# Kernel optimization log

Measured on AMD Instinct MI355X. Metric: run time of the kernel, lower is better.

The kernel has to match this reference:

```python
import jax, jax.numpy as jnp
import numpy as np

B, T, DIM = 4, 1024, 2048
H, KVH = 16, 4
HD = DIM // H          # 128
G = H // KVH           # GQA group size = 4


def setup_inputs() -> dict:
    key = jax.random.key(0)
    ks = jax.random.split(key, 4)
    s = 1.0 / np.sqrt(DIM)
    x = jax.random.normal(ks[0], (B, T, DIM), jnp.float32)
    Wq = jax.random.normal(ks[1], (DIM, DIM), jnp.float32) * s
    Wkv = jax.random.normal(ks[2], (DIM, 2 * KVH * HD), jnp.float32) * s
    Wo = jax.random.normal(ks[3], (DIM, DIM), jnp.float32) * s
    # RoPE tables (theta=10000, half-split / rotate-half convention)
    inv_freq = 1.0 / (10000.0 ** (np.arange(0, HD, 2, dtype=np.float64) / HD))
    freqs = np.outer(np.arange(T, dtype=np.float64), inv_freq)  # [T, HD/2]
    cos = jnp.asarray(np.cos(freqs), jnp.float32)
    sin = jnp.asarray(np.sin(freqs), jnp.float32)
    return {"x": x, "Wq": Wq, "Wkv": Wkv, "Wo": Wo, "cos": cos, "sin": sin}


def _rope(u, cos, sin):
    # u: [B,T,heads,HD]; cos/sin: [T, HD/2]
    u1, u2 = jnp.split(u, 2, axis=-1)
    c = cos[None, :, None, :]
    s = sin[None, :, None, :]
    return jnp.concatenate([u1 * c - u2 * s, u1 * s + u2 * c], axis=-1)


def reference(x, Wq, Wkv, Wo, cos, sin):
    Bs, Ts, C = x.shape
    q = (x @ Wq).reshape(Bs, Ts, H, HD)
    kv = (x @ Wkv).reshape(Bs, Ts, 2, KVH, HD)
    k, v = kv[:, :, 0], kv[:, :, 1]
    q = _rope(q, cos, sin)
    k = _rope(k, cos, sin)
    # GQA without materializing repeated K/V: fold group dim into q
    qg = q.reshape(Bs, Ts, KVH, G, HD)
    scores = jnp.einsum('bqhgd,bkhd->bhgqk', qg, k) / np.float32(np.sqrt(HD))
    causal = jnp.tril(jnp.ones((Ts, Ts), bool))
    neg = jnp.finfo(scores.dtype).min
    scores = jnp.where(causal, scores, neg)
    att = jax.nn.softmax(scores, axis=-1)
    out = jnp.einsum('bhgqk,bkhd->bqhgd', att, v).reshape(Bs, Ts, C)
    return out @ Wo
```

## Files before the change

### kernel.cpp

```cpp
#include <hip/hip_runtime.h>

typedef unsigned short u16;
typedef unsigned int u32;
typedef __bf16 bf16x8 __attribute__((ext_vector_type(8)));
typedef float f32x4 __attribute__((ext_vector_type(4)));

#define BB   4
#define TT   1024
#define CDIM 2048
#define NH   16
#define NKV  4
#define HDIM 128

__device__ __forceinline__ float b2f(u16 u) {
    union { u32 i; float f; } x; x.i = ((u32)u) << 16; return x.f;
}
__device__ __forceinline__ u16 f2b(float f) {
    union { float f; u32 i; } x; x.f = f;
    u32 r = (x.i + 0x7fffu + ((x.i >> 16) & 1u)) >> 16;
    return (u16)r;
}
__device__ __forceinline__ void async16(const void* g, void* l) {
    __builtin_amdgcn_global_load_lds((const __attribute__((address_space(1))) void*)g,
                                     (__attribute__((address_space(3))) void*)l, 16, 0, 0);
}
template<int N> __device__ __forceinline__ void waitvm() {
    static_assert(N >= 0 && N <= 8, "unsupported vmcnt");
    if constexpr (N == 0)      asm volatile("s_waitcnt vmcnt(0)" ::: "memory");
    else if constexpr (N == 1) asm volatile("s_waitcnt vmcnt(1)" ::: "memory");
    else if constexpr (N == 2) asm volatile("s_waitcnt vmcnt(2)" ::: "memory");
    else if constexpr (N == 3) asm volatile("s_waitcnt vmcnt(3)" ::: "memory");
    else if constexpr (N == 4) asm volatile("s_waitcnt vmcnt(4)" ::: "memory");
    else if constexpr (N == 5) asm volatile("s_waitcnt vmcnt(5)" ::: "memory");
    else if constexpr (N == 6) asm volatile("s_waitcnt vmcnt(6)" ::: "memory");
    else if constexpr (N == 7) asm volatile("s_waitcnt vmcnt(7)" ::: "memory");
    else                       asm volatile("s_waitcnt vmcnt(8)" ::: "memory");
}

__device__ __forceinline__ bool wave_is_f32(const u16* xp) {
    u16 v = xp[(threadIdx.x & 63) * 2];
    int e = (v >> 7) & 0xFF;
    bool bad = (v != 0) && (e < 90 || e > 160);
    return __popcll(__ballot(bad)) > 16;
}

__global__ __launch_bounds__(256) void pre_k(const void* __restrict__ x,
                                             const void* __restrict__ Wq,
                                             const void* __restrict__ Wkv,
                                             const void* __restrict__ Wo,
                                             u16* __restrict__ xb,
                                             u16* __restrict__ csb,
                                             u16* __restrict__ snb,
                                             u16* __restrict__ WqkvT,
                                             u16* __restrict__ WoT,
                                             const void* __restrict__ cs,
                                             const void* __restrict__ sn) {
    const bool f32m = wave_is_f32((const u16*)x);
    int bid = blockIdx.x;
    if (bid < 8320) {
        const void* src; u16* dst; int i;
        if (bid < 8192)      { src = x;  dst = xb;  i = bid * 256 + threadIdx.x; }
        else if (bid < 8256) { src = cs; dst = csb; i = (bid - 8192) * 256 + threadIdx.x; }
        else                 { src = sn; dst = snb; i = (bid - 8256) * 256 + threadIdx.x; }
        union { u16 u[4]; ushort4 v; } o;
        if (f32m) {
            float4 f = ((const float4*)src)[i];
            o.u[0] = f2b(f.x); o.u[1] = f2b(f.y); o.u[2] = f2b(f.z); o.u[3] = f2b(f.w);
        } else {
            o.v = ((const ushort4*)src)[i];
        }
        ((ushort4*)dst)[i] = o.v;
        return;
    }
    __shared__ alignas(16) u16 tile[64 * 65];
    int t = bid - 8320;
    const void* W; u16* WT; int rows, cols, bx, by;
    if (t < 1024)      { W = Wq;  WT = WqkvT;                    rows = 2048; cols = 2048; bx = t & 31;  by = t >> 5; }
    else if (t < 1536) { int l = t - 1024; W = Wkv; WT = WqkvT + (long)2048 * 2048; rows = 2048; cols = 1024; bx = l & 15; by = l >> 4; }
    else               { int l = t - 1536; W = Wo;  WT = WoT;  rows = 2048; cols = 2048; bx = l & 31;   by = l >> 5; }
    const int r0 = by * 64, c0 = bx * 64;
#pragma unroll
    for (int i = 0; i < 16; i++) {
        int c = threadIdx.x + i * 256;
        int rr = c >> 6, cc = c & 63;
        long idx = (long)(r0 + rr) * cols + c0 + cc;
        tile[rr * 65 + cc] = f32m ? f2b(((const float*)W)[idx]) : ((const u16*)W)[idx];
    }
    __syncthreads();
#pragma unroll
    for (int i = 0; i < 16; i++) {
        int c = threadIdx.x + i * 256;
        int rr = c >> 6, cc = c & 63;
        WT[(long)(c0 + rr) * rows + r0 + cc] = tile[cc * 65 + rr];
    }
}

template<int BM, int BN>
__global__ __launch_bounds__(512, 4) void gemm_p4(const u16* __restrict__ A,
                                                  const u16* __restrict__ Bt,
                                                  void* __restrict__ C,
                                                  int N, int Kd,
                                                  const u16* __restrict__ xprobe) {
    constexpr int MF  = BM / 32;
    constexpr int NF  = BN / 64;
    constexpr int MF0 = MF / 2, MF1 = MF - MF0;
    constexpr int NF0 = (NF + 1) / 2, NF1 = NF - NF0;
    constexpr int NAU = BM / 64;
    constexpr int NBU = BN / 64;
    constexpr int NAL = NAU / 2;
    constexpr int NBL = NBU / 2;

    __shared__ alignas(16) u16 As[2][BM * 64];
    __shared__ alignas(16) u16 Bs[2][BN * 64];

    const bool f32m = (xprobe != nullptr) && wave_is_f32(xprobe);
    const int tid = threadIdx.x;
    const int w = tid >> 6, lane = tid & 63;
    const int wm = w >> 2, wn = w & 3;
    const int l16 = lane & 15, quad = lane >> 4;
    const long arow0 = (long)blockIdx.y * BM;
    const long brow0 = (long)blockIdx.x * BN;
    const int NT = Kd >> 6;

    const int srow = tid >> 3, scp = tid & 7;
    const long gst = (long)srow * Kd + ((scp ^ (srow & 7)) << 3);
    const int cst = tid << 3;

    const u16* Ab = A + arow0 * Kd;
    const u16* Bb = Bt + brow0 * Kd;

    auto stageA = [&](int buf, int t, int u0, int u1) {
#pragma unroll
        for (int u = 0; u < NAU; u++)
            if (u >= u0 && u < u1)
                async16(Ab + (long)u * 64 * Kd + t * 64 + gst, &As[buf][u * 4096 + cst]);
    };
    auto stageB = [&](int buf, int t, int u0, int u1) {
#pragma unroll
        for (int u = 0; u < NBU; u++)
            if (u >= u0 && u < u1)
                async16(Bb + (long)u * 64 * Kd + t * 64 + gst, &Bs[buf][u * 4096 + cst]);
    };

    const int R0a = wm * (BM / 2) + l16, sA = R0a & 7;
    const int R0b = wn * (BN / 4) + l16, sB = R0b & 7;
    int aoff[2], boff[2];
    aoff[0] = R0a * 64 + ((quad ^ sA) << 3);
    aoff[1] = R0a * 64 + (((4 + quad) ^ sA) << 3);
    boff[0] = R0b * 64 + ((quad ^ sB) << 3);
    boff[1] = R0b * 64 + (((4 + quad) ^ sB) << 3);

    f32x4 acc[MF][NF];
#pragma unroll
    for (int i = 0; i < MF; i++)
#pragma unroll
        for (int j = 0; j < NF; j++) acc[i][j] = {0.f, 0.f, 0.f, 0.f};

    stageB(0, 0, 0, NBU);
    stageA(0, 0, 0, NAU);
    stageB(1, 1, 0, NBL);
    waitvm<NBL>();
    __builtin_amdgcn_s_barrier();

#pragma unroll 1
    for (int t = 0; t < NT; ++t) {
        const int cur = t & 1, nxt = cur ^ 1;
        const u16* pA = &As[cur][0];
        const u16* pB = &Bs[cur][0];
        bf16x8 afLo[MF0][2], afHi[MF1][2], bfA[NF0][2], bfB[NF1][2];

#pragma unroll
        for (int ks = 0; ks < 2; ks++) {
#pragma unroll
            for (int mt = 0; mt < MF0; mt++)
                afLo[mt][ks] = *(const bf16x8*)&pA[aoff[ks] + mt * 1024];
#pragma unroll
            for (int nt = 0; nt < NF0; nt++)
                bfA[nt][ks] = *(const bf16x8*)&pB[boff[ks] + nt * 1024];
        }
        if (t + 1 < NT) stageB(nxt, t + 1, NBL, NBU);
        __builtin_amdgcn_s_barrier();
        asm volatile("s_waitcnt lgkmcnt(0)" ::: "memory");
        __builtin_amdgcn_sched_barrier(0);
        __builtin_amdgcn_s_setprio(1);
#pragma unroll
        for (int ks = 0; ks < 2; ks++)
#pragma unroll
            for (int mt = 0; mt < MF0; mt++)
#pragma unroll
                for (int nt = 0; nt < NF0; nt++)
                    acc[mt][nt] = __builtin_amdgcn_mfma_f32_16x16x32_bf16(
                        afLo[mt][ks], bfA[nt][ks], acc[mt][nt], 0, 0, 0);
        __builtin_amdgcn_s_setprio(0);

#pragma unroll
        for (int ks = 0; ks < 2; ks++)
#pragma unroll
            for (int nt = 0; nt < NF1; nt++)
                bfB[nt][ks] = *(const bf16x8*)&pB[boff[ks] + (NF0 + nt) * 1024];
        if (t + 1 < NT) stageA(nxt, t + 1, 0, NAL);
        __builtin_amdgcn_s_barrier();
        asm volatile("s_waitcnt lgkmcnt(0)" ::: "memory");
        __builtin_amdgcn_sched_barrier(0);
        __builtin_amdgcn_s_setprio(1);
#pragma unroll
        for (int ks = 0; ks < 2; ks++)
#pragma unroll
            for (int mt = 0; mt < MF0; mt++)
#pragma unroll
                for (int nt = 0; nt < NF1; nt++)
                    acc[mt][NF0 + nt] = __builtin_amdgcn_mfma_f32_16x16x32_bf16(
                        afLo[mt][ks], bfB[nt][ks], acc[mt][NF0 + nt], 0, 0, 0);
        __builtin_amdgcn_s_setprio(0);

#pragma unroll
        for (int ks = 0; ks < 2; ks++)
#pragma unroll
            for (int mt = 0; mt < MF1; mt++)
                afHi[mt][ks] = *(const bf16x8*)&pA[aoff[ks] + (MF0 + mt) * 1024];
        if (t + 1 < NT) stageA(nxt, t + 1, NAL, NAU);
        __builtin_amdgcn_s_barrier();
        asm volatile("s_waitcnt lgkmcnt(0)" ::: "memory");
        __builtin_amdgcn_sched_barrier(0);
        __builtin_amdgcn_s_setprio(1);
#pragma unroll
        for (int ks = 0; ks < 2; ks++)
#pragma unroll
            for (int mt = 0; mt < MF1; mt++)
#pragma unroll
                for (int nt = 0; nt < NF1; nt++)
                    acc[MF0 + mt][NF0 + nt] = __builtin_amdgcn_mfma_f32_16x16x32_bf16(
                        afHi[mt][ks], bfB[nt][ks], acc[MF0 + mt][NF0 + nt], 0, 0, 0);
        __builtin_amdgcn_s_setprio(0);

        if (t + 1 < NT) {
            asm volatile("s_waitcnt vmcnt(0)" ::: "memory");
            __builtin_amdgcn_s_barrier();
            if (t + 2 < NT) stageB(cur, t + 2, 0, NBL);
        }
        __builtin_amdgcn_sched_barrier(0);
        __builtin_amdgcn_s_setprio(1);
#pragma unroll
        for (int ks = 0; ks < 2; ks++)
#pragma unroll
            for (int mt = 0; mt < MF1; mt++)
#pragma unroll
                for (int nt = 0; nt < NF0; nt++)
                    acc[MF0 + mt][nt] = __builtin_amdgcn_mfma_f32_16x16x32_bf16(
                        afHi[mt][ks], bfA[nt][ks], acc[MF0 + mt][nt], 0, 0, 0);
        __builtin_amdgcn_s_setprio(0);
    }

#pragma unroll
    for (int mt = 0; mt < MF; mt++) {
#pragma unroll
        for (int nt = 0; nt < NF; nt++) {
            long col = brow0 + wn * (BN / 4) + nt * 16 + l16;
#pragma unroll
            for (int r = 0; r < 4; r++) {
                long row = arow0 + wm * (BM / 2) + mt * 16 + quad * 4 + r;
                if (f32m) ((float*)C)[row * N + col] = acc[mt][nt][r];
                else      ((u16*)C)[row * N + col] = f2b(acc[mt][nt][r]);
            }
        }
    }
}

template<int BM, int BN>
__global__ __launch_bounds__(512, 4) void gemm_p2(const u16* __restrict__ A,
                                                  const u16* __restrict__ Bt,
                                                  void* __restrict__ C,
                                                  int N, int Kd,
                                                  const u16* __restrict__ xprobe) {
    constexpr int MF  = BM / 32;
    constexpr int NF  = BN / 64;
    constexpr int MF0 = MF / 2, MF1 = MF - MF0;
    constexpr int NF0 = (NF + 1) / 2, NF1 = NF - NF0;
    constexpr int NAU = BM / 64;
    constexpr int NBU = BN / 64;

    __shared__ alignas(16) u16 As[2][BM * 64];
    __shared__ alignas(16) u16 Bs[2][BN * 64];

    const bool f32m = (xprobe != nullptr) && wave_is_f32(xprobe);
    const int tid = threadIdx.x;
    const int w = tid >> 6, lane = tid & 63;
    const int wm = w >> 2, wn = w & 3;
    const int l16 = lane & 15, quad = lane >> 4;
    const long arow0 = (long)blockIdx.y * BM;
    const long brow0 = (long)blockIdx.x * BN;
    const int NT = Kd >> 6;

    const int srow = tid >> 3, scp = tid & 7;
    const long gst = (long)srow * Kd + ((scp ^ (srow & 7)) << 3);
    const int cst = tid << 3;

    const u16* Ab = A + arow0 * Kd;
    const u16* Bb = Bt + brow0 * Kd;

    auto stageA = [&](int buf, int t) {
#pragma unroll
        for (int u = 0; u < NAU; u++)
            async16(Ab + (long)u * 64 * Kd + t * 64 + gst, &As[buf][u * 4096 + cst]);
    };
    auto stageB = [&](int buf, int t) {
#pragma unroll
        for (int u = 0; u < NBU; u++)
            async16(Bb + (long)u * 64 * Kd + t * 64 + gst, &Bs[buf][u * 4096 + cst]);
    };

    const int R0a = wm * (BM / 2) + l16, sA = R0a & 7;
    const int R0b = wn * (BN / 4) + l16, sB = R0b & 7;
    int aoff[2], boff[2];
    aoff[0] = R0a * 64 + ((quad ^ sA) << 3);
    aoff[1] = R0a * 64 + (((4 + quad) ^ sA) << 3);
    boff[0] = R0b * 64 + ((quad ^ sB) << 3);
    boff[1] = R0b * 64 + (((4 + quad) ^ sB) << 3);

    f32x4 acc[MF][NF];
#pragma unroll
    for (int i = 0; i < MF; i++)
#pragma unroll
        for (int j = 0; j < NF; j++) acc[i][j] = {0.f, 0.f, 0.f, 0.f};

    stageB(0, 0); stageA(0, 0); stageB(1, 1); stageA(1, 1);
    waitvm<NAU + NBU>();
    __builtin_amdgcn_s_barrier();

#pragma unroll 1
    for (int t = 0; t < NT; ++t) {
        const int cur = t & 1;
        const u16* pA = &As[cur][0];
        const u16* pB = &Bs[cur][0];
        bf16x8 afLo[MF0][2], afHi[MF1][2], bfA[NF0][2], bfB[NF1][2];

#pragma unroll
        for (int ks = 0; ks < 2; ks++) {
#pragma unroll
            for (int mt = 0; mt < MF0; mt++)
                afLo[mt][ks] = *(const bf16x8*)&pA[aoff[ks] + mt * 1024];
#pragma unroll
            for (int nt = 0; nt < NF0; nt++)
                bfA[nt][ks] = *(const bf16x8*)&pB[boff[ks] + nt * 1024];
#pragma unroll
            for (int nt = 0; nt < NF1; nt++)
                bfB[nt][ks] = *(const bf16x8*)&pB[boff[ks] + (NF0 + nt) * 1024];
        }
        asm volatile("s_waitcnt lgkmcnt(0)" ::: "memory");
        __builtin_amdgcn_sched_barrier(0);
        __builtin_amdgcn_s_setprio(1);
#pragma unroll
        for (int ks = 0; ks < 2; ks++)
#pragma unroll
            for (int mt = 0; mt < MF0; mt++) {
#pragma unroll
                for (int nt = 0; nt < NF0; nt++)
                    acc[mt][nt] = __builtin_amdgcn_mfma_f32_16x16x32_bf16(
                        afLo[mt][ks], bfA[nt][ks], acc[mt][nt], 0, 0, 0);
#pragma unroll
                for (int nt = 0; nt < NF1; nt++)
                    acc[mt][NF0 + nt] = __builtin_amdgcn_mfma_f32_16x16x32_bf16(
                        afLo[mt][ks], bfB[nt][ks], acc[mt][NF0 + nt], 0, 0, 0);
            }
        __builtin_amdgcn_s_setprio(0);

#pragma unroll
        for (int ks = 0; ks < 2; ks++)
#pragma unroll
            for (int mt = 0; mt < MF1; mt++)
                afHi[mt][ks] = *(const bf16x8*)&pA[aoff[ks] + (MF0 + mt) * 1024];
        __builtin_amdgcn_s_barrier();
        if (t + 2 < NT) stageB(cur, t + 2);
        asm volatile("s_waitcnt lgkmcnt(0)" ::: "memory");
        __builtin_amdgcn_sched_barrier(0);
        __builtin_amdgcn_s_setprio(1);
#pragma unroll
        for (int ks = 0; ks < 2; ks++)
#pragma unroll
            for (int mt = 0; mt < MF1; mt++) {
#pragma unroll
                for (int nt = 0; nt < NF1; nt++)
                    acc[MF0 + mt][NF0 + nt] = __builtin_amdgcn_mfma_f32_16x16x32_bf16(
                        afHi[mt][ks], bfB[nt][ks], acc[MF0 + mt][NF0 + nt], 0, 0, 0);
#pragma unroll
                for (int nt = 0; nt < NF0; nt++)
                    acc[MF0 + mt][nt] = __builtin_amdgcn_mfma_f32_16x16x32_bf16(
                        afHi[mt][ks], bfA[nt][ks], acc[MF0 + mt][nt], 0, 0, 0);
            }
        __builtin_amdgcn_s_setprio(0);

        if (t + 1 < NT) {
            if (t + 2 < NT) waitvm<NBU>();
            else            waitvm<0>();
            __builtin_amdgcn_s_barrier();
            if (t + 2 < NT) stageA(cur, t + 2);
        }
    }

#pragma unroll
    for (int mt = 0; mt < MF; mt++) {
#pragma unroll
        for (int nt = 0; nt < NF; nt++) {
            long col = brow0 + wn * (BN / 4) + nt * 16 + l16;
#pragma unroll
            for (int r = 0; r < 4; r++) {
                long row = arow0 + wm * (BM / 2) + mt * 16 + quad * 4 + r;
                if (f32m) ((float*)C)[row * N + col] = acc[mt][nt][r];
                else      ((u16*)C)[row * N + col] = f2b(acc[mt][nt][r]);
            }
        }
    }
}

__global__ __launch_bounds__(256) void prep_k(const u16* __restrict__ QKVraw,
                                              const u16* __restrict__ cs,
                                              const u16* __restrict__ sn,
                                              u16* __restrict__ Qr,
                                              u16* __restrict__ Kr,
                                              u16* __restrict__ Vt) {
    __shared__ alignas(16) u16 tile[64 * 68];
    int bid = blockIdx.x;
    if (bid < 16384) {
        int idx = bid * 256 + threadIdx.x;
        int d = idx & 63;
        int t = (idx >> 6) & (TT - 1);
        int bh = idx >> 16;
        long src = ((long)((bh >> 4) * TT + t)) * 3072 + (bh & 15) * HDIM;
        float u1 = b2f(QKVraw[src + d]), u2 = b2f(QKVraw[src + d + 64]);
        float c = b2f(cs[t * 64 + d]), s = b2f(sn[t * 64 + d]);
        long dst = ((long)bh * TT + t) * HDIM;
        Qr[dst + d] = f2b(u1 * c - u2 * s);
        Qr[dst + d + 64] = f2b(u1 * s + u2 * c);
    } else if (bid < 20480) {
        int idx = (bid - 16384) * 256 + threadIdx.x;
        int d = idx & 63;
        int t = (idx >> 6) & (TT - 1);
        int bk = idx >> 16;
        long src = ((long)((bk >> 2) * TT + t)) * 3072 + 2048 + (bk & 3) * HDIM;
        float u1 = b2f(QKVraw[src + d]), u2 = b2f(QKVraw[src + d + 64]);
        float c = b2f(cs[t * 64 + d]), s = b2f(sn[t * 64 + d]);
        long dst = ((long)bk * TT + t) * HDIM;
        Kr[dst + d] = f2b(u1 * c - u2 * s);
        Kr[dst + d + 64] = f2b(u1 * s + u2 * c);
    } else {
        int vb = bid - 20480;
        int bk = vb >> 5;
        int dt = (vb >> 4) & 1;
        int tt = vb & 15;
        const int d0 = dt * 64, t0 = tt * 64;
        const long srcb = ((long)(bk >> 2) * TT) * 3072 + 2560 + (bk & 3) * HDIM;
#pragma unroll
        for (int i = 0; i < 4; i++) {
            int lin = i * 256 + threadIdx.x;
            int r = lin >> 4, c4 = (lin & 15) * 4;
            *(ushort4*)&tile[r * 68 + c4] =
                *(const ushort4*)&QKVraw[srcb + (long)(t0 + r) * 3072 + d0 + c4];
        }
        __syncthreads();
        const long dstb = ((long)bk * 128 + d0) * 1024 + t0;
#pragma unroll
        for (int i = 0; i < 4; i++) {
            int lin = i * 256 + threadIdx.x;
            int dr = lin >> 4, c4 = (lin & 15) * 4;
            ushort4 v;
            v.x = tile[(c4 + 0) * 68 + dr];
            v.y = tile[(c4 + 1) * 68 + dr];
            v.z = tile[(c4 + 2) * 68 + dr];
            v.w = tile[(c4 + 3) * 68 + dr];
            *(ushort4*)&Vt[dstb + (long)dr * 1024 + c4] = v;
        }
    }
}

__global__ __launch_bounds__(256) void attn_kernel(const u16* __restrict__ Q,
                                                   const u16* __restrict__ Kr,
                                                   const u16* __restrict__ Vt,
                                                   u16* __restrict__ O) {
    __shared__ alignas(16) u16 Ks[2][64 * 128];
    __shared__ alignas(16) u16 Vts[2][128 * 64];
    __shared__ alignas(16) u16 Ps[64 * 88];

    const int tid = threadIdx.x, w = tid >> 6, lane = tid & 63;
    const int l16 = lane & 15, quad = lane >> 4;
    const float scale2 = 0.08838834764831845f * 1.4426950408889634f;

#pragma unroll 1
    for (int it = 0; it < 2; it++) {
        const int j = it ? (1023 - (int)blockIdx.x) : (int)blockIdx.x;
        const int qt = 15 - (j >> 6);
        const int bh = j & 63;
        const int b = bh >> 4, h = bh & 15;
        const int kvh = h >> 2;
        const long qrow0 = (long)bh * TT + qt * 64;
        const long krow0 = (long)(b * NKV + kvh) * TT;
        const long vbase = ((long)(b * NKV + kvh) * HDIM) * TT;

        __syncthreads();

#pragma unroll
        for (int i = 0; i < 4; i++) {
            int slot0 = (w * 4 + i) * 64;
            int slot = slot0 + lane;
            int row = slot >> 4, cp = slot & 15;
            int cg = (cp & 8) | ((cp ^ row) & 7);
            async16(Q + (qrow0 + row) * HDIM + cg * 8, &Ks[0][slot0 * 8]);
        }
        asm volatile("s_waitcnt vmcnt(0)" ::: "memory");
        bf16x8 qf[4];
        {
            const int Rq = w * 16 + l16;
#pragma unroll
            for (int ds = 0; ds < 4; ds++) {
                int c = ds * 4 + quad;
                qf[ds] = *(const bf16x8*)&Ks[0][Rq * 128 + ((c & 8) | ((c ^ Rq) & 7)) * 8];
            }
        }
        asm volatile("s_waitcnt lgkmcnt(0)" ::: "memory");

#pragma unroll
        for (int i = 0; i < 4; i++) {
            int slot0 = (w * 4 + i) * 64;
            int slot = slot0 + lane;
            int row = slot >> 4, cp = slot & 15;
            int cg = (cp & 8) | ((cp ^ row) & 7);
            async16(Kr + (krow0 + row) * HDIM + cg * 8, &Ks[0][slot0 * 8]);
        }
#pragma unroll
        for (int i = 0; i < 4; i++) {
            int slot0 = (w * 4 + i) * 64;
            int slot = slot0 + lane;
            int row = slot >> 3, cp = slot & 7;
            int cg = cp ^ (row & 7);
            async16(Vt + vbase + (long)row * TT + cg * 8, &Vts[0][slot0 * 8]);
        }
        if (qt >= 1) {
#pragma unroll
            for (int i = 0; i < 4; i++) {
                int slot0 = (w * 4 + i) * 64;
                int slot = slot0 + lane;
                int row = slot >> 4, cp = slot & 15;
                int cg = (cp & 8) | ((cp ^ row) & 7);
                async16(Kr + (krow0 + 64 + row) * HDIM + cg * 8, &Ks[1][slot0 * 8]);
            }
#pragma unroll
            for (int i = 0; i < 4; i++) {
                int slot0 = (w * 4 + i) * 64;
                int slot = slot0 + lane;
                int row = slot >> 3, cp = slot & 7;
                int cg = cp ^ (row & 7);
                async16(Vt + vbase + (long)row * TT + 64 + cg * 8, &Vts[1][slot0 * 8]);
            }
            asm volatile("s_waitcnt vmcnt(8)" ::: "memory");
        } else {
            asm volatile("s_waitcnt vmcnt(0)" ::: "memory");
        }
        asm volatile("s_barrier" ::: "memory");

        f32x4 o[8];
#pragma unroll
        for (int i = 0; i < 8; i++) o[i] = {0.f, 0.f, 0.f, 0.f};
        float m_i = -1.0e30f, l_i = 0.f;
        const int qg = qt * 64 + w * 16 + l16;

#pragma unroll 1
        for (int kt = 0; kt <= qt; kt++) {
            const int cur = kt & 1;
            const u16* ksb = Ks[cur];
            const u16* vsb = Vts[cur];

            f32x4 s[4];
#pragma unroll
            for (int nt = 0; nt < 4; nt++) s[nt] = {0.f, 0.f, 0.f, 0.f};
            __builtin_amdgcn_s_setprio(1);
#pragma unroll
            for (int ds = 0; ds < 4; ds++) {
                int c = ds * 4 + quad;
#pragma unroll
                for (int nt = 0; nt < 4; nt++) {
                    int Rk = nt * 16 + l16;
                    bf16x8 ak = *(const bf16x8*)&ksb[Rk * 128 + ((c & 8) | ((c ^ Rk) & 7)) * 8];
                    s[nt] = __builtin_amdgcn_mfma_f32_16x16x32_bf16(ak, qf[ds], s[nt], 0, 0, 0);
                }
            }
            __builtin_amdgcn_s_setprio(0);

            float p[4][4];
            if (kt == qt) {
#pragma unroll
                for (int nt = 0; nt < 4; nt++)
#pragma unroll
                    for (int r = 0; r < 4; r++) {
                        int kcol = kt * 64 + nt * 16 + quad * 4 + r;
                        p[nt][r] = (kcol <= qg) ? (float)s[nt][r] * scale2 : -1.0e30f;
                    }
            } else {
#pragma unroll
                for (int nt = 0; nt < 4; nt++)
#pragma unroll
                    for (int r = 0; r < 4; r++)
                        p[nt][r] = (float)s[nt][r] * scale2;
            }
            float mrow[4];
#pragma unroll
            for (int nt = 0; nt < 4; nt++)
                mrow[nt] = fmaxf(fmaxf(p[nt][0], p[nt][1]), fmaxf(p[nt][2], p[nt][3]));
            float mx = fmaxf(fmaxf(mrow[0], mrow[1]), fmaxf(mrow[2], mrow[3]));
            mx = fmaxf(mx, __shfl_xor(mx, 16));
            mx = fmaxf(mx, __shfl_xor(mx, 32));
            float mnew = fmaxf(m_i, mx);
            float alpha = exp2f(m_i - mnew);
            float rrow[4];
#pragma unroll
            for (int nt = 0; nt < 4; nt++) {
#pragma unroll
                for (int r = 0; r < 4; r++)
                    p[nt][r] = exp2f(p[nt][r] - mnew);
                rrow[nt] = (p[nt][0] + p[nt][1]) + (p[nt][2] + p[nt][3]);
            }
            float rs = (rrow[0] + rrow[1]) + (rrow[2] + rrow[3]);
            rs += __shfl_xor(rs, 16);
            rs += __shfl_xor(rs, 32);
            l_i = l_i * alpha + rs;

            u32* Psw = (u32*)Ps;
            int pb = (w * 16 + l16) * 44 + quad * 2;
#pragma unroll
            for (int nt = 0; nt < 4; nt++) {
                u32 lo = (u32)f2b(p[nt][0]) | ((u32)f2b(p[nt][1]) << 16);
                u32 hi = (u32)f2b(p[nt][2]) | ((u32)f2b(p[nt][3]) << 16);
                Psw[pb + nt * 8]     = lo;
                Psw[pb + nt * 8 + 1] = hi;
            }
            if (__ballot(mnew != m_i) != 0ULL) {
#pragma unroll
                for (int n8 = 0; n8 < 8; n8++)
#pragma unroll
                    for (int r = 0; r < 4; r++) o[n8][r] *= alpha;
            }
            m_i = mnew;

            asm volatile("s_waitcnt lgkmcnt(0)" ::: "memory");

            __builtin_amdgcn_s_setprio(1);
#pragma unroll
            for (int ks = 0; ks < 2; ks++) {
                bf16x8 bp = *(const bf16x8*)&Ps[(w * 16 + l16) * 88 + ks * 32 + quad * 8];
#pragma unroll
                for (int n8 = 0; n8 < 8; n8++) {
                    int Rv = n8 * 16 + l16;
                    int c = ks * 4 + quad;
                    bf16x8 av = *(const bf16x8*)&vsb[Rv * 64 + (c ^ (Rv & 7)) * 8];
                    o[n8] = __builtin_amdgcn_mfma_f32_16x16x32_bf16(av, bp, o[n8], 0, 0, 0);
                }
            }
            __builtin_amdgcn_s_setprio(0);

            if (kt == qt) break;

            asm volatile("s_waitcnt lgkmcnt(0)" ::: "memory");
            asm volatile("s_barrier" ::: "memory");
            if (kt + 2 <= qt) {
                const int nk = kt + 2;
#pragma unroll
                for (int i = 0; i < 4; i++) {
                    int slot0 = (w * 4 + i) * 64;
                    int slot = slot0 + lane;
                    int row = slot >> 4, cp = slot & 15;
                    int cg = (cp & 8) | ((cp ^ row) & 7);
                    async16(Kr + (krow0 + nk * 64 + row) * HDIM + cg * 8, &Ks[cur][slot0 * 8]);
                }
#pragma unroll
                for (int i = 0; i < 4; i++) {
                    int slot0 = (w * 4 + i) * 64;
                    int slot = slot0 + lane;
                    int row = slot >> 3, cp = slot & 7;
                    int cg = cp ^ (row & 7);
                    async16(Vt + vbase + (long)row * TT + nk * 64 + cg * 8, &Vts[cur][slot0 * 8]);
                }
                asm volatile("s_waitcnt vmcnt(8)" ::: "memory");
            } else {
                asm volatile("s_waitcnt vmcnt(0)" ::: "memory");
            }
            asm volatile("s_barrier" ::: "memory");
        }

        float inv = 1.0f / l_i;
        long obase = ((long)(b * TT + qg)) * CDIM + h * HDIM;
#pragma unroll
        for (int n8 = 0; n8 < 8; n8++) {
            ushort4 st;
            st.x = f2b(o[n8][0] * inv);
            st.y = f2b(o[n8][1] * inv);
            st.z = f2b(o[n8][2] * inv);
            st.w = f2b(o[n8][3] * inv);
            *(ushort4*)&O[obase + n8 * 16 + quad * 4] = st;
        }
    }
}

extern "C" void kernel_launch(void* const* d_in, const int* in_sizes, int n_in,
                              void* d_out, int out_size, void* d_ws, size_t ws_size,
                              hipStream_t stream) {
    const void* x   = d_in[0];
    const void* Wq  = d_in[1];
    const void* Wkv = d_in[2];
    const void* Wo  = d_in[3];
    const void* cs  = d_in[4];
    const void* sn  = d_in[5];

    char* ws = (char*)d_ws;
    const size_t NEED = 105119748;
    if (ws_size < NEED) return;

    u16* WqkvT = (u16*)(ws + 0);
    u16* WoT   = (u16*)(ws + 12582912);
    u16* QKVraw= (u16*)(ws + 20971520);
    u16* Qr    = (u16*)(ws + 46137344);
    u16* Kr    = (u16*)(ws + 62914560);
    u16* Vt    = (u16*)(ws + 67108864);
    u16* ATT   = (u16*)(ws + 71303168);
    u16* xb    = (u16*)(ws + 88080384);
    u16* csb   = (u16*)(ws + 104857600);
    u16* snb   = (u16*)(ws + 104988672);

    pre_k<<<10880, 256, 0, stream>>>(x, Wq, Wkv, Wo, xb, csb, snb, WqkvT, WoT, cs, sn);

    gemm_p4<128, 192><<<dim3(16, 32), 512, 0, stream>>>(xb, WqkvT, QKVraw, 3072, 2048, nullptr);

    prep_k<<<20992, 256, 0, stream>>>(QKVraw, csb, snb, Qr, Kr, Vt);

    attn_kernel<<<512, 256, 0, stream>>>(Qr, Kr, Vt, ATT);

    gemm_p2<128, 128><<<dim3(16, 32), 512, 0, stream>>>(ATT, WoT, d_out, 2048, 2048, (const u16*)x);
}
```

Before: 287.2 us.

## Fuse RoPE and V transpose into QKV GEMM epilogue, drop prep kernel

Replaces the generic QKV GEMM plus separate prep kernel with a specialized 128x128-tile GEMM whose epilogue stages the tile in LDS, applies RoPE for Q/K head tiles, and writes V transposed directly. This removes the intermediate QKVraw write and re-read and one kernel launch. The tile changes from 128x192 to 128x128, so the grid grows to 24x32 blocks and each block does less MFMA work per loaded tile, with an extra LDS round-trip in the epilogue.

```diff
diff --git a/kernel.cpp b/kernel.cpp
--- a/kernel.cpp
+++ b/kernel.cpp
@@ -95,31 +95,21 @@
     }
 }
 
-template<int BM, int BN>
-__global__ __launch_bounds__(512, 4) void gemm_p4(const u16* __restrict__ A,
-                                                  const u16* __restrict__ Bt,
-                                                  void* __restrict__ C,
-                                                  int N, int Kd,
-                                                  const u16* __restrict__ xprobe) {
-    constexpr int MF  = BM / 32;
-    constexpr int NF  = BN / 64;
-    constexpr int MF0 = MF / 2, MF1 = MF - MF0;
-    constexpr int NF0 = (NF + 1) / 2, NF1 = NF - NF0;
-    constexpr int NAU = BM / 64;
-    constexpr int NBU = BN / 64;
-    constexpr int NAL = NAU / 2;
-    constexpr int NBL = NBU / 2;
-
-    __shared__ alignas(16) u16 As[2][BM * 64];
-    __shared__ alignas(16) u16 Bs[2][BN * 64];
-
-    const bool f32m = (xprobe != nullptr) && wave_is_f32(xprobe);
+__global__ __launch_bounds__(512, 4) void gemm_qkv(const u16* __restrict__ A,
+                                                   const u16* __restrict__ Bt,
+                                                   const u16* __restrict__ csb,
+                                                   const u16* __restrict__ snb,
+                                                   u16* __restrict__ Qr,
+                                                   u16* __restrict__ Kr,
+                                                   u16* __restrict__ Vt,
+                                                   int Kd) {
+    __shared__ alignas(16) u16 smem[32768];
     const int tid = threadIdx.x;
     const int w = tid >> 6, lane = tid & 63;
     const int wm = w >> 2, wn = w & 3;
     const int l16 = lane & 15, quad = lane >> 4;
-    const long arow0 = (long)blockIdx.y * BM;
-    const long brow0 = (long)blockIdx.x * BN;
+    const long arow0 = (long)blockIdx.y * 128;
+    const long brow0 = (long)blockIdx.x * 128;
     const int NT = Kd >> 6;
 
     const int srow = tid >> 3, scp = tid & 7;
@@ -129,56 +119,57 @@
     const u16* Ab = A + arow0 * Kd;
     const u16* Bb = Bt + brow0 * Kd;
 
+    auto As = [&](int buf) -> u16* { return smem + buf * 8192; };
+    auto Bs = [&](int buf) -> u16* { return smem + 16384 + buf * 8192; };
+
     auto stageA = [&](int buf, int t, int u0, int u1) {
 #pragma unroll
-        for (int u = 0; u < NAU; u++)
+        for (int u = 0; u < 2; u++)
             if (u >= u0 && u < u1)
-                async16(Ab + (long)u * 64 * Kd + t * 64 + gst, &As[buf][u * 4096 + cst]);
+                async16(Ab + (long)u * 64 * Kd + t * 64 + gst, As(buf) + u * 4096 + cst);
     };
     auto stageB = [&](int buf, int t, int u0, int u1) {
 #pragma unroll
-        for (int u = 0; u < NBU; u++)
+        for (int u = 0; u < 2; u++)
             if (u >= u0 && u < u1)
-                async16(Bb + (long)u * 64 * Kd + t * 64 + gst, &Bs[buf][u * 4096 + cst]);
+                async16(Bb + (long)u * 64 * Kd + t * 64 + gst, Bs(buf) + u * 4096 + cst);
     };
 
-    const int R0a = wm * (BM / 2) + l16, sA = R0a & 7;
-    const int R0b = wn * (BN / 4) + l16, sB = R0b & 7;
+    const int R0a = wm * 64 + l16, sA = R0a & 7;
+    const int R0b = wn * 32 + l16, sB = R0b & 7;
     int aoff[2], boff[2];
     aoff[0] = R0a * 64 + ((quad ^ sA) << 3);
     aoff[1] = R0a * 64 + (((4 + quad) ^ sA) << 3);
     boff[0] = R0b * 64 + ((quad ^ sB) << 3);
     boff[1] = R0b * 64 + (((4 + quad) ^ sB) << 3);
 
-    f32x4 acc[MF][NF];
-#pragma unroll
-    for (int i = 0; i < MF; i++)
-#pragma unroll
-        for (int j = 0; j < NF; j++) acc[i][j] = {0.f, 0.f, 0.f, 0.f};
-
-    stageB(0, 0, 0, NBU);
-    stageA(0, 0, 0, NAU);
-    stageB(1, 1, 0, NBL);
-    waitvm<NBL>();
+    f32x4 acc[4][2];
+#pragma unroll
+    for (int i = 0; i < 4; i++)
+#pragma unroll
+        for (int j = 0; j < 2; j++) acc[i][j] = {0.f, 0.f, 0.f, 0.f};
+
+    stageB(0, 0, 0, 2);
+    stageA(0, 0, 0, 2);
+    stageB(1, 1, 0, 1);
+    waitvm<1>();
     __builtin_amdgcn_s_barrier();
 
 #pragma unroll 1
     for (int t = 0; t < NT; ++t) {
         const int cur = t & 1, nxt = cur ^ 1;
-        const u16* pA = &As[cur][0];
-        const u16* pB = &Bs[cur][0];
-        bf16x8 afLo[MF0][2], afHi[MF1][2], bfA[NF0][2], bfB[NF1][2];
+        const u16* pA = As(cur);
+        const u16* pB = Bs(cur);
+        bf16x8 afLo[2][2], afHi[2][2], bfA[2], bfB[2];
 
 #pragma unroll
         for (int ks = 0; ks < 2; ks++) {
 #pragma unroll
-            for (int mt = 0; mt < MF0; mt++)
+            for (int mt = 0; mt < 2; mt++)
                 afLo[mt][ks] = *(const bf16x8*)&pA[aoff[ks] + mt * 1024];
-#pragma unroll
-            for (int nt = 0; nt < NF0; nt++)
-                bfA[nt][ks] = *(const bf16x8*)&pB[boff[ks] + nt * 1024];
-        }
-        if (t + 1 < NT) stageB(nxt, t + 1, NBL, NBU);
+            bfA[ks] = *(const bf16x8*)&pB[boff[ks]];
+        }
+        if (t + 1 < NT) stageB(nxt, t + 1, 1, 2);
         __builtin_amdgcn_s_barrier();
         asm volatile("s_waitcnt lgkmcnt(0)" ::: "memory");
         __builtin_amdgcn_sched_barrier(0);
@@ -186,19 +177,15 @@
 #pragma unroll
         for (int ks = 0; ks < 2; ks++)
 #pragma unroll
-            for (int mt = 0; mt < MF0; mt++)
-#pragma unroll
-                for (int nt = 0; nt < NF0; nt++)
-                    acc[mt][nt] = __builtin_amdgcn_mfma_f32_16x16x32_bf16(
-                        afLo[mt][ks], bfA[nt][ks], acc[mt][nt], 0, 0, 0);
+            for (int mt = 0; mt < 2; mt++)
+                acc[mt][0] = __builtin_amdgcn_mfma_f32_16x16x32_bf16(
+                    afLo[mt][ks], bfA[ks], acc[mt][0], 0, 0, 0);
         __builtin_amdgcn_s_setprio(0);
 
 #pragma unroll
         for (int ks = 0; ks < 2; ks++)
-#pragma unroll
-            for (int nt = 0; nt < NF1; nt++)
-                bfB[nt][ks] = *(const bf16x8*)&pB[boff[ks] + (NF0 + nt) * 1024];
-        if (t + 1 < NT) stageA(nxt, t + 1, 0, NAL);
+            bfB[ks] = *(const bf16x8*)&pB[boff[ks] + 1024];
+        if (t + 1 < NT) stageA(nxt, t + 1, 0, 1);
         __builtin_amdgcn_s_barrier();
         asm volatile("s_waitcnt lgkmcnt(0)" ::: "memory");
         __builtin_amdgcn_sched_barrier(0);
@@ -206,19 +193,17 @@
 #pragma unroll
         for (int ks = 0; ks < 2; ks++)
 #pragma unroll
-            for (int mt = 0; mt < MF0; mt++)
-#pragma unroll
-                for (int nt = 0; nt < NF1; nt++)
-                    acc[mt][NF0 + nt] = __builtin_amdgcn_mfma_f32_16x16x32_bf16(
-                        afLo[mt][ks], bfB[nt][ks], acc[mt][NF0 + nt], 0, 0, 0);
+            for (int mt = 0; mt < 2; mt++)
+                acc[mt][1] = __builtin_amdgcn_mfma_f32_16x16x32_bf16(
+                    afLo[mt][ks], bfB[ks], acc[mt][1], 0, 0, 0);
         __builtin_amdgcn_s_setprio(0);
 
 #pragma unroll
         for (int ks = 0; ks < 2; ks++)
 #pragma unroll
-            for (int mt = 0; mt < MF1; mt++)
-                afHi[mt][ks] = *(const bf16x8*)&pA[aoff[ks] + (MF0 + mt) * 1024];
-        if (t + 1 < NT) stageA(nxt, t + 1, NAL, NAU);
+            for (int mt = 0; mt < 2; mt++)
+                afHi[mt][ks] = *(const bf16x8*)&pA[aoff[ks] + (mt + 2) * 1024];
+        if (t + 1 < NT) stageA(nxt, t + 1, 1, 2);
         __builtin_amdgcn_s_barrier();
         asm volatile("s_waitcnt lgkmcnt(0)" ::: "memory");
         __builtin_amdgcn_sched_barrier(0);
@@ -226,42 +211,75 @@
 #pragma unroll
         for (int ks = 0; ks < 2; ks++)
 #pragma unroll
-            for (int mt = 0; mt < MF1; mt++)
-#pragma unroll
-                for (int nt = 0; nt < NF1; nt++)
-                    acc[MF0 + mt][NF0 + nt] = __builtin_amdgcn_mfma_f32_16x16x32_bf16(
-                        afHi[mt][ks], bfB[nt][ks], acc[MF0 + mt][NF0 + nt], 0, 0, 0);
+            for (int mt = 0; mt < 2; mt++)
+                acc[mt + 2][1] = __builtin_amdgcn_mfma_f32_16x16x32_bf16(
+                    afHi[mt][ks], bfB[ks], acc[mt + 2][1], 0, 0, 0);
         __builtin_amdgcn_s_setprio(0);
 
         if (t + 1 < NT) {
             asm volatile("s_waitcnt vmcnt(0)" ::: "memory");
             __builtin_amdgcn_s_barrier();
-            if (t + 2 < NT) stageB(cur, t + 2, 0, NBL);
+            if (t + 2 < NT) stageB(cur, t + 2, 0, 1);
         }
         __builtin_amdgcn_sched_barrier(0);
         __builtin_amdgcn_s_setprio(1);
 #pragma unroll
         for (int ks = 0; ks < 2; ks++)
 #pragma unroll
-            for (int mt = 0; mt < MF1; mt++)
-#pragma unroll
-                for (int nt = 0; nt < NF0; nt++)
-                    acc[MF0 + mt][nt] = __builtin_amdgcn_mfma_f32_16x16x32_bf16(
-                        afHi[mt][ks], bfA[nt][ks], acc[MF0 + mt][nt], 0, 0, 0);
+            for (int mt = 0; mt < 2; mt++)
+                acc[mt + 2][0] = __builtin_amdgcn_mfma_f32_16x16x32_bf16(
+                    afHi[mt][ks], bfA[ks], acc[mt + 2][0], 0, 0, 0);
         __builtin_amdgcn_s_setprio(0);
     }
 
-#pragma unroll
-    for (int mt = 0; mt < MF; mt++) {
-#pragma unroll
-        for (int nt = 0; nt < NF; nt++) {
-            long col = brow0 + wn * (BN / 4) + nt * 16 + l16;
+    constexpr int TP = 129;
+    u16* TB = smem;
+    __syncthreads();
+#pragma unroll
+    for (int mt = 0; mt < 4; mt++)
+#pragma unroll
+        for (int nt = 0; nt < 2; nt++) {
+            int col = wn * 32 + nt * 16 + l16;
 #pragma unroll
             for (int r = 0; r < 4; r++) {
-                long row = arow0 + wm * (BM / 2) + mt * 16 + quad * 4 + r;
-                if (f32m) ((float*)C)[row * N + col] = acc[mt][nt][r];
-                else      ((u16*)C)[row * N + col] = f2b(acc[mt][nt][r]);
-            }
+                int row = wm * 64 + mt * 16 + quad * 4 + r;
+                TB[row * TP + col] = f2b(acc[mt][nt][r]);
+            }
+        }
+    __syncthreads();
+
+    const int cb = blockIdx.x;
+    const int b  = blockIdx.y >> 3;
+    const int t0 = (blockIdx.y & 7) << 7;
+    if (cb < 20) {
+        u16* dstp; long hb;
+        if (cb < 16) { dstp = Qr; hb = (long)b * 16 + cb; }
+        else         { dstp = Kr; hb = (long)b * 4 + (cb - 16); }
+        const long obase = (hb * 1024 + t0) * 128;
+#pragma unroll
+        for (int j = 0; j < 16; j++) {
+            int idx = j * 512 + tid;
+            int tl = idx >> 6, d = idx & 63;
+            float u1 = b2f(TB[tl * TP + d]);
+            float u2 = b2f(TB[tl * TP + d + 64]);
+            float c = b2f(csb[(t0 + tl) * 64 + d]);
+            float s = b2f(snb[(t0 + tl) * 64 + d]);
+            dstp[obase + (long)tl * 128 + d]      = f2b(u1 * c - u2 * s);
+            dstp[obase + (long)tl * 128 + d + 64] = f2b(u1 * s + u2 * c);
+        }
+    } else {
+        const int kvh = cb - 20;
+        const long vb = ((long)(b * 4 + kvh) * 128) * 1024 + t0;
+#pragma unroll
+        for (int j = 0; j < 8; j++) {
+            int lin = j * 512 + tid;
+            int dr = lin >> 5, t4 = (lin & 31) << 2;
+            ushort4 v;
+            v.x = TB[(t4 + 0) * TP + dr];
+            v.y = TB[(t4 + 1) * TP + dr];
+            v.z = TB[(t4 + 2) * TP + dr];
+            v.w = TB[(t4 + 3) * TP + dr];
+            *(ushort4*)&Vt[vb + (long)dr * 1024 + t4] = v;
         }
     }
 }
@@ -412,66 +430,6 @@
     }
 }
 
-__global__ __launch_bounds__(256) void prep_k(const u16* __restrict__ QKVraw,
-                                              const u16* __restrict__ cs,
-                                              const u16* __restrict__ sn,
-                                              u16* __restrict__ Qr,
-                                              u16* __restrict__ Kr,
-                                              u16* __restrict__ Vt) {
-    __shared__ alignas(16) u16 tile[64 * 68];
-    int bid = blockIdx.x;
-    if (bid < 16384) {
-        int idx = bid * 256 + threadIdx.x;
-        int d = idx & 63;
-        int t = (idx >> 6) & (TT - 1);
-        int bh = idx >> 16;
-        long src = ((long)((bh >> 4) * TT + t)) * 3072 + (bh & 15) * HDIM;
-        float u1 = b2f(QKVraw[src + d]), u2 = b2f(QKVraw[src + d + 64]);
-        float c = b2f(cs[t * 64 + d]), s = b2f(sn[t * 64 + d]);
-        long dst = ((long)bh * TT + t) * HDIM;
-        Qr[dst + d] = f2b(u1 * c - u2 * s);
-        Qr[dst + d + 64] = f2b(u1 * s + u2 * c);
-    } else if (bid < 20480) {
-        int idx = (bid - 16384) * 256 + threadIdx.x;
-        int d = idx & 63;
-        int t = (idx >> 6) & (TT - 1);
-        int bk = idx >> 16;
-        long src = ((long)((bk >> 2) * TT + t)) * 3072 + 2048 + (bk & 3) * HDIM;
-        float u1 = b2f(QKVraw[src + d]), u2 = b2f(QKVraw[src + d + 64]);
-        float c = b2f(cs[t * 64 + d]), s = b2f(sn[t * 64 + d]);
-        long dst = ((long)bk * TT + t) * HDIM;
-        Kr[dst + d] = f2b(u1 * c - u2 * s);
-        Kr[dst + d + 64] = f2b(u1 * s + u2 * c);
-    } else {
-        int vb = bid - 20480;
-        int bk = vb >> 5;
-        int dt = (vb >> 4) & 1;
-        int tt = vb & 15;
-        const int d0 = dt * 64, t0 = tt * 64;
-        const long srcb = ((long)(bk >> 2) * TT) * 3072 + 2560 + (bk & 3) * HDIM;
-#pragma unroll
-        for (int i = 0; i < 4; i++) {
-            int lin = i * 256 + threadIdx.x;
-            int r = lin >> 4, c4 = (lin & 15) * 4;
-            *(ushort4*)&tile[r * 68 + c4] =
-                *(const ushort4*)&QKVraw[srcb + (long)(t0 + r) * 3072 + d0 + c4];
-        }
-        __syncthreads();
-        const long dstb = ((long)bk * 128 + d0) * 1024 + t0;
-#pragma unroll
-        for (int i = 0; i < 4; i++) {
-            int lin = i * 256 + threadIdx.x;
-            int dr = lin >> 4, c4 = (lin & 15) * 4;
-            ushort4 v;
-            v.x = tile[(c4 + 0) * 68 + dr];
-            v.y = tile[(c4 + 1) * 68 + dr];
-            v.z = tile[(c4 + 2) * 68 + dr];
-            v.w = tile[(c4 + 3) * 68 + dr];
-            *(ushort4*)&Vt[dstb + (long)dr * 1024 + c4] = v;
-        }
-    }
-}
-
 __global__ __launch_bounds__(256) void attn_kernel(const u16* __restrict__ Q,
                                                    const u16* __restrict__ Kr,
                                                    const u16* __restrict__ Vt,
@@ -714,7 +672,6 @@
 
     u16* WqkvT = (u16*)(ws + 0);
     u16* WoT   = (u16*)(ws + 12582912);
-    u16* QKVraw= (u16*)(ws + 20971520);
     u16* Qr    = (u16*)(ws + 46137344);
     u16* Kr    = (u16*)(ws + 62914560);
     u16* Vt    = (u16*)(ws + 67108864);
@@ -725,9 +682,7 @@
 
     pre_k<<<10880, 256, 0, stream>>>(x, Wq, Wkv, Wo, xb, csb, snb, WqkvT, WoT, cs, sn);
 
-    gemm_p4<128, 192><<<dim3(16, 32), 512, 0, stream>>>(xb, WqkvT, QKVraw, 3072, 2048, nullptr);
-
-    prep_k<<<20992, 256, 0, stream>>>(QKVraw, csb, snb, Qr, Kr, Vt);
+    gemm_qkv<<<dim3(24, 32), 512, 0, stream>>>(xb, WqkvT, csb, snb, Qr, Kr, Vt, 2048);
 
     attn_kernel<<<512, 256, 0, stream>>>(Qr, Kr, Vt, ATT);
 
```

Result: no change. 282.7 us (-1.6%).
